# Performance work log

Hardware: AMD Instinct MI355X
Metric: run time of the kernel (lower is better)

The kernel has to match this reference:

```python
import jax, jax.numpy as jnp
import numpy as np


def setup_inputs() -> dict:
    key = jax.random.key(0)
    k1, k2 = jax.random.split(key)
    T, K, D = 100000, 512, 64
    flags_matrix = jax.random.uniform(k1, (T, K), dtype=jnp.float32)  # ~half > 0.5
    emb_weight = jax.random.normal(k2, (K, D), dtype=jnp.float32)
    return {"flags_matrix": flags_matrix, "emb_weight": emb_weight}


def reference(flags_matrix, emb_weight):
    # mask[t,k] = 1 if flag active; bag-of-embeddings mean over active items per row.
    mask = (flags_matrix > 0.5).astype(emb_weight.dtype)          # [T, K]
    counts = jnp.sum(mask, axis=1, keepdims=True)                  # [T, 1]
    sums = mask @ emb_weight                                       # [T, D] masked sum of embeddings
    # rows with no active flags -> zeros (matches the torch branch)
    return jnp.where(counts > 0, sums / jnp.maximum(counts, 1.0), 0.0)
```

## Files before the change

### kernel.cpp

```cpp
#include <hip/hip_runtime.h>
#include <stdint.h>


#define T_ROWS 100000
#define K_FLAGS 512
#define D_DIM 64
#define TILES (T_ROWS / 16)

typedef __attribute__((ext_vector_type(4))) float f32x4;
typedef __attribute__((ext_vector_type(8))) short bf16x8;

__device__ __forceinline__ uint32_t f32_to_bf16_rne(float f) {
  union { float f; uint32_t u; } v; v.f = f;
  uint32_t u = v.u;
  return (u + 0x7FFFu + ((u >> 16) & 1u)) >> 16;
}

__global__ __launch_bounds__(1024, 8) void flagbag_kernel(const float* __restrict__ flags,
                                                          const float* __restrict__ W,
                                                          float* __restrict__ out) {
  __shared__ uint4 sB[16 * 4 * 64];
  __shared__ uint32_t sM[16][256];

  const int tid  = threadIdx.x;
  const int lane = tid & 63;
  const int wave = tid >> 6;
  const int tile = wave * 512 + (int)blockIdx.x;
  const bool active = (tile < TILES);
  const int t0 = tile * 16;

  if (active) {
    const float* ft = flags + (size_t)t0 * K_FLAGS + lane * 8;

    uint32_t D0 = 0, D1 = 0, D2 = 0, D3 = 0;
    f32x4 ra[4], rb[4];
#pragma unroll
    for (int r = 0; r < 3; ++r) {
      ra[r] = *reinterpret_cast<const f32x4*>(ft + r * K_FLAGS);
      rb[r] = *reinterpret_cast<const f32x4*>(ft + r * K_FLAGS + 4);
    }
#pragma unroll
    for (int r = 0; r < 16; ++r) {
      if (r + 3 < 16) {
        ra[(r + 3) & 3] = *reinterpret_cast<const f32x4*>(ft + (r + 3) * K_FLAGS);
        rb[(r + 3) & 3] = *reinterpret_cast<const f32x4*>(ft + (r + 3) * K_FLAGS + 4);
      }
      const f32x4 a = ra[r & 3], b = rb[r & 3];
      uint32_t byte = 0;
#pragma unroll
      for (int j = 0; j < 4; ++j) {
        byte |= (a[j] > 0.5f) ? (1u << j)       : 0u;
        byte |= (b[j] > 0.5f) ? (1u << (j + 4)) : 0u;
      }
      const uint32_t sh = byte << ((r & 3) * 8);
      if ((r >> 2) == 0) D0 |= sh;
      else if ((r >> 2) == 1) D1 |= sh;
      else if ((r >> 2) == 2) D2 |= sh;
      else D3 |= sh;
    }

    uint32_t* sMw = sM[wave];
    sMw[0 * 64 + (lane ^ 0)]  = D0;
    sMw[1 * 64 + (lane ^ 4)]  = D1;
    sMw[2 * 64 + (lane ^ 8)]  = D2;
    sMw[3 * 64 + (lane ^ 12)] = D3;
  }

#pragma unroll
  for (int p = 0; p < 4; ++p) {
    const int E  = tid + p * 1024;
    const int s  = E >> 8;
    const int nt = (E >> 6) & 3;
    const int ln = E & 63;
    const int n  = (ln & 15) + 16 * nt;
    const int kq = ln >> 4;
    const int kb = 128 * kq + 8 * s;
    uint32_t r[4];
#pragma unroll
    for (int j = 0; j < 4; ++j) {
      uint32_t lo = f32_to_bf16_rne(W[(size_t)(kb + 2 * j    ) * D_DIM + n]);
      uint32_t hi = f32_to_bf16_rne(W[(size_t)(kb + 2 * j + 1) * D_DIM + n]);
      r[j] = lo | (hi << 16);
    }
    sB[E] = make_uint4(r[0], r[1], r[2], r[3]);
  }
  __syncthreads();

  if (!active) return;

  const int m  = lane & 15;
  const int kq = lane >> 4;
  const int mj = m >> 2, mb = m & 3;
  const uint8_t* sMb = reinterpret_cast<const uint8_t*>(sM[wave]);

  uint32_t mbytes[16];
#pragma unroll
  for (int s = 0; s < 16; ++s)
    mbytes[s] = sMb[(size_t)(mj * 64 + ((16 * kq + s) ^ (4 * mj))) * 4 + mb];

  int cnt = 0;
#pragma unroll
  for (int s = 0; s < 16; ++s) cnt += __popc(mbytes[s]);
  cnt += __shfl_xor(cnt, 16);
  cnt += __shfl_xor(cnt, 32);
  const float inv = (cnt > 0) ? (1.0f / (float)cnt) : 0.0f;

  const uint4* sbl = &sB[lane];
  f32x4 acc[4];
#pragma unroll
  for (int nt = 0; nt < 4; ++nt) acc[nt] = (f32x4){0.f, 0.f, 0.f, 0.f};

  uint4 bc[4], bn[4];
#pragma unroll
  for (int nt = 0; nt < 4; ++nt) bc[nt] = sbl[nt * 64];

#pragma unroll
  for (int s = 0; s < 16; ++s) {
    if (s + 1 < 16) {
#pragma unroll
      for (int nt = 0; nt < 4; ++nt) bn[nt] = sbl[((s + 1) * 4 + nt) * 64];
    }
    const uint32_t byte = mbytes[s];
    bf16x8 af;
#pragma unroll
    for (int e = 0; e < 8; ++e) af[e] = ((byte >> e) & 1u) ? (short)0x3F80 : (short)0;

#pragma unroll
    for (int nt = 0; nt < 4; ++nt)
      acc[nt] = __builtin_amdgcn_mfma_f32_16x16x32_bf16(
          af, *reinterpret_cast<const bf16x8*>(&bc[nt]), acc[nt], 0, 0, 0);

#pragma unroll
    for (int nt = 0; nt < 4; ++nt) bc[nt] = bn[nt];
  }

#pragma unroll
  for (int r = 0; r < 4; ++r) {
    const int row = kq * 4 + r;
    const float invr = __shfl(inv, row);
    float* orow = out + (size_t)(t0 + row) * D_DIM + m;
#pragma unroll
    for (int nt = 0; nt < 4; ++nt)
      orow[16 * nt] = acc[nt][r] * invr;
  }
}

extern "C" void kernel_launch(void* const* d_in, const int* in_sizes, int n_in,
                              void* d_out, int out_size, void* d_ws, size_t ws_size,
                              hipStream_t stream) {
  const float* flags = (const float*)d_in[0];
  const float* W     = (const float*)d_in[1];
  float* out         = (float*)d_out;

  hipLaunchKernelGGL(flagbag_kernel, dim3(512), dim3(1024), 0, stream, flags, W, out);
}
```

Before: 42.95 us.

## Switch to 32x32x16 MFMA with wave pairs sharing 32-row tiles

Replaces the per-wave 16-row tile computed with four 16x16x32 MFMAs per k-step with 32-row tiles split across wave pairs. Each wave builds masks for 16 rows, and each wave of the pair computes one 32-column half of the output using 32 steps of the 32x32x16 bf16 MFMA. This cuts per-wave accumulator registers and LDS B-fragment loads, and reorganises the swizzled shared mask and B layouts to match. Count reduction and output writes are remapped to the 32x32 accumulator layout. The trade-off is more serial MFMA steps per wave and shared dependence between waves of a pair through the mask buffer.

Measured after the change: 47.31 us. 1.1x slower.

```diff
diff --git a/kernel.cpp b/kernel.cpp
--- a/kernel.cpp
+++ b/kernel.cpp
@@ -5,10 +5,11 @@
 #define T_ROWS 100000
 #define K_FLAGS 512
 #define D_DIM 64
-#define TILES (T_ROWS / 16)
+#define TILES32 (T_ROWS / 32)
 
-typedef __attribute__((ext_vector_type(4))) float f32x4;
-typedef __attribute__((ext_vector_type(8))) short bf16x8;
+typedef __attribute__((ext_vector_type(4)))  float f32x4;
+typedef __attribute__((ext_vector_type(16))) float f32x16;
+typedef __attribute__((ext_vector_type(8)))  short bf16x8;
 
 __device__ __forceinline__ uint32_t f32_to_bf16_rne(float f) {
   union { float f; uint32_t u; } v; v.f = f;
@@ -19,18 +20,20 @@
 __global__ __launch_bounds__(1024, 8) void flagbag_kernel(const float* __restrict__ flags,
                                                           const float* __restrict__ W,
                                                           float* __restrict__ out) {
-  __shared__ uint4 sB[16 * 4 * 64];
-  __shared__ uint32_t sM[16][256];
+  __shared__ uint4 sB[32 * 2 * 64];
+  __shared__ uint32_t sM[8][512];
 
-  const int tid  = threadIdx.x;
-  const int lane = tid & 63;
-  const int wave = tid >> 6;
-  const int tile = wave * 512 + (int)blockIdx.x;
-  const bool active = (tile < TILES);
-  const int t0 = tile * 16;
+  const int tid   = threadIdx.x;
+  const int lane  = tid & 63;
+  const int wave  = tid >> 6;
+  const int pairv = wave >> 1;
+  const int mate  = wave & 1;
+  const int slot  = pairv * 512 + (int)blockIdx.x;
+  const bool active = (slot < TILES32);
+  const int t0 = (active ? slot : 0) * 32;
 
   if (active) {
-    const float* ft = flags + (size_t)t0 * K_FLAGS + lane * 8;
+    const float* ft = flags + (size_t)(t0 + 16 * mate) * K_FLAGS + lane * 8;
 
     uint32_t D0 = 0, D1 = 0, D2 = 0, D3 = 0;
     f32x4 ra[4], rb[4];
@@ -59,22 +62,22 @@
       else D3 |= sh;
     }
 
-    uint32_t* sMw = sM[wave];
-    sMw[0 * 64 + (lane ^ 0)]  = D0;
-    sMw[1 * 64 + (lane ^ 4)]  = D1;
-    sMw[2 * 64 + (lane ^ 8)]  = D2;
-    sMw[3 * 64 + (lane ^ 12)] = D3;
+    uint32_t* sMp = sM[pairv];
+    const int xr = 16 * mate;
+    sMp[mate * 256 + 0 * 64 + (lane ^ 0  ^ xr)] = D0;
+    sMp[mate * 256 + 1 * 64 + (lane ^ 4  ^ xr)] = D1;
+    sMp[mate * 256 + 2 * 64 + (lane ^ 8  ^ xr)] = D2;
+    sMp[mate * 256 + 3 * 64 + (lane ^ 12 ^ xr)] = D3;
   }
 
 #pragma unroll
   for (int p = 0; p < 4; ++p) {
-    const int E  = tid + p * 1024;
-    const int s  = E >> 8;
-    const int nt = (E >> 6) & 3;
-    const int ln = E & 63;
-    const int n  = (ln & 15) + 16 * nt;
-    const int kq = ln >> 4;
-    const int kb = 128 * kq + 8 * s;
+    const int E   = tid + p * 1024;
+    const int ln  = E & 63;
+    const int ntc = (E >> 6) & 1;
+    const int s   = E >> 7;
+    const int n   = (ln & 31) + 32 * ntc;
+    const int kb  = 16 * s + 8 * (ln >> 5);
     uint32_t r[4];
 #pragma unroll
     for (int j = 0; j < 4; ++j) {
@@ -85,63 +88,48 @@
     sB[E] = make_uint4(r[0], r[1], r[2], r[3]);
   }
   __syncthreads();
-
   if (!active) return;
 
-  const int m  = lane & 15;
-  const int kq = lane >> 4;
-  const int mj = m >> 2, mb = m & 3;
-  const uint8_t* sMb = reinterpret_cast<const uint8_t*>(sM[wave]);
+  const int lr     = lane & 31;
+  const int kg     = lane >> 5;
+  const int region = lr >> 4;
+  const int mj     = (lr & 15) >> 2;
+  const int mb     = lr & 3;
+  const int baseDw = region * 256 + mj * 64;
+  const int X      = (4 * mj) ^ (16 * region);
+  const uint8_t* sMb = reinterpret_cast<const uint8_t*>(sM[pairv]);
 
-  uint32_t mbytes[16];
+  f32x16 acc;
 #pragma unroll
-  for (int s = 0; s < 16; ++s)
-    mbytes[s] = sMb[(size_t)(mj * 64 + ((16 * kq + s) ^ (4 * mj))) * 4 + mb];
+  for (int i = 0; i < 16; ++i) acc[i] = 0.f;
+  int cnt = 0;
 
-  int cnt = 0;
+  uint4 bc = sB[mate * 64 + lane];
 #pragma unroll
-  for (int s = 0; s < 16; ++s) cnt += __popc(mbytes[s]);
-  cnt += __shfl_xor(cnt, 16);
-  cnt += __shfl_xor(cnt, 32);
-  const float inv = (cnt > 0) ? (1.0f / (float)cnt) : 0.0f;
+  for (int s = 0; s < 32; ++s) {
+    uint4 bn;
+    if (s + 1 < 32) bn = sB[(s + 1) * 128 + mate * 64 + lane];
 
-  const uint4* sbl = &sB[lane];
-  f32x4 acc[4];
-#pragma unroll
-  for (int nt = 0; nt < 4; ++nt) acc[nt] = (f32x4){0.f, 0.f, 0.f, 0.f};
+    const uint32_t byte = sMb[(size_t)(baseDw + ((2 * s + kg) ^ X)) * 4 + mb];
+    cnt += __popc(byte);
 
-  uint4 bc[4], bn[4];
-#pragma unroll
-  for (int nt = 0; nt < 4; ++nt) bc[nt] = sbl[nt * 64];
-
-#pragma unroll
-  for (int s = 0; s < 16; ++s) {
-    if (s + 1 < 16) {
-#pragma unroll
-      for (int nt = 0; nt < 4; ++nt) bn[nt] = sbl[((s + 1) * 4 + nt) * 64];
-    }
-    const uint32_t byte = mbytes[s];
     bf16x8 af;
 #pragma unroll
     for (int e = 0; e < 8; ++e) af[e] = ((byte >> e) & 1u) ? (short)0x3F80 : (short)0;
 
-#pragma unroll
-    for (int nt = 0; nt < 4; ++nt)
-      acc[nt] = __builtin_amdgcn_mfma_f32_16x16x32_bf16(
-          af, *reinterpret_cast<const bf16x8*>(&bc[nt]), acc[nt], 0, 0, 0);
+    acc = __builtin_amdgcn_mfma_f32_32x32x16_bf16(
+        af, *reinterpret_cast<const bf16x8*>(&bc), acc, 0, 0, 0);
+    bc = bn;
+  }
+
+  cnt += __shfl_xor(cnt, 32);
+  const float inv = (cnt > 0) ? (1.0f / (float)cnt) : 0.0f;
 
 #pragma unroll
-    for (int nt = 0; nt < 4; ++nt) bc[nt] = bn[nt];
-  }
-
-#pragma unroll
-  for (int r = 0; r < 4; ++r) {
-    const int row = kq * 4 + r;
+  for (int reg = 0; reg < 16; ++reg) {
+    const int row = (reg & 3) + 8 * (reg >> 2) + 4 * kg;
     const float invr = __shfl(inv, row);
-    float* orow = out + (size_t)(t0 + row) * D_DIM + m;
-#pragma unroll
-    for (int nt = 0; nt < 4; ++nt)
-      orow[16 * nt] = acc[nt][r] * invr;
+    out[(size_t)(t0 + row) * D_DIM + lr + 32 * mate] = acc[reg] * invr;
   }
 }
 
```

## Pair waves to share mask tiles and split output columns

Applied to the files above, without the earlier changes.

Waves are paired over a 32-row slot. Each wave still packs the flag bits for its own 16 rows. After the barrier, each wave computes both 16-row tiles but only half of the 64 output columns. This halves the per-wave LDS reads of the bf16 embedding fragments, at the cost of reading mask bytes from two LDS slabs and building two A fragments per step. Row counts are now accumulated inside the MFMA loop. The kernel reads about 200 MB of flags, so it is likely bound by HBM bandwidth, which caps any gain.

Result: slower. 47.85 us (+11.4%).

```diff
diff --git a/kernel.cpp b/kernel.cpp
--- a/kernel.cpp
+++ b/kernel.cpp
@@ -5,7 +5,7 @@
 #define T_ROWS 100000
 #define K_FLAGS 512
 #define D_DIM 64
-#define TILES (T_ROWS / 16)
+#define TILES32 (T_ROWS / 32)
 
 typedef __attribute__((ext_vector_type(4))) float f32x4;
 typedef __attribute__((ext_vector_type(8))) short bf16x8;
@@ -25,12 +25,14 @@
   const int tid  = threadIdx.x;
   const int lane = tid & 63;
   const int wave = tid >> 6;
-  const int tile = wave * 512 + (int)blockIdx.x;
-  const bool active = (tile < TILES);
-  const int t0 = tile * 16;
+  const int pair = wave >> 1;
+  const int mate = wave & 1;
+  const int slot = pair * 512 + (int)blockIdx.x;
+  const bool active = (slot < TILES32);
+  const int t0 = (active ? slot : 0) * 32;
 
   if (active) {
-    const float* ft = flags + (size_t)t0 * K_FLAGS + lane * 8;
+    const float* ft = flags + (size_t)(t0 + 16 * mate) * K_FLAGS + lane * 8;
 
     uint32_t D0 = 0, D1 = 0, D2 = 0, D3 = 0;
     f32x4 ra[4], rb[4];
@@ -73,8 +75,7 @@
     const int nt = (E >> 6) & 3;
     const int ln = E & 63;
     const int n  = (ln & 15) + 16 * nt;
-    const int kq = ln >> 4;
-    const int kb = 128 * kq + 8 * s;
+    const int kb = 128 * (ln >> 4) + 8 * s;
     uint32_t r[4];
 #pragma unroll
     for (int j = 0; j < 4; ++j) {
@@ -85,63 +86,70 @@
     sB[E] = make_uint4(r[0], r[1], r[2], r[3]);
   }
   __syncthreads();
-
   if (!active) return;
 
   const int m  = lane & 15;
   const int kq = lane >> 4;
   const int mj = m >> 2, mb = m & 3;
-  const uint8_t* sMb = reinterpret_cast<const uint8_t*>(sM[wave]);
+  const int m4 = 4 * mj;
+  const int C  = 4 * (mj * 64 + 16 * kq) + mb;
+  const uint8_t* sA0 = reinterpret_cast<const uint8_t*>(sM[pair * 2    ]);
+  const uint8_t* sA1 = reinterpret_cast<const uint8_t*>(sM[pair * 2 + 1]);
+  const int ntb = 2 * mate;
 
-  uint32_t mbytes[16];
-#pragma unroll
-  for (int s = 0; s < 16; ++s)
-    mbytes[s] = sMb[(size_t)(mj * 64 + ((16 * kq + s) ^ (4 * mj))) * 4 + mb];
+  f32x4 a00 = {0.f,0.f,0.f,0.f}, a01 = {0.f,0.f,0.f,0.f};
+  f32x4 a10 = {0.f,0.f,0.f,0.f}, a11 = {0.f,0.f,0.f,0.f};
+  int cntA = 0, cntB = 0;
 
-  int cnt = 0;
-#pragma unroll
-  for (int s = 0; s < 16; ++s) cnt += __popc(mbytes[s]);
-  cnt += __shfl_xor(cnt, 16);
-  cnt += __shfl_xor(cnt, 32);
-  const float inv = (cnt > 0) ? (1.0f / (float)cnt) : 0.0f;
-
-  const uint4* sbl = &sB[lane];
-  f32x4 acc[4];
-#pragma unroll
-  for (int nt = 0; nt < 4; ++nt) acc[nt] = (f32x4){0.f, 0.f, 0.f, 0.f};
-
-  uint4 bc[4], bn[4];
-#pragma unroll
-  for (int nt = 0; nt < 4; ++nt) bc[nt] = sbl[nt * 64];
+  uint4 bc0 = sB[ntb * 64 + lane];
+  uint4 bc1 = sB[(ntb + 1) * 64 + lane];
 
 #pragma unroll
   for (int s = 0; s < 16; ++s) {
+    uint4 bn0, bn1;
     if (s + 1 < 16) {
+      bn0 = sB[(s + 1) * 256 + ntb * 64 + lane];
+      bn1 = sB[(s + 1) * 256 + (ntb + 1) * 64 + lane];
+    }
+
+    const uint32_t byteA = sA0[C + 4 * (s ^ m4)];
+    const uint32_t byteB = sA1[C + 4 * (s ^ m4)];
+    cntA += __popc(byteA);
+    cntB += __popc(byteB);
+
+    bf16x8 afA, afB;
 #pragma unroll
-      for (int nt = 0; nt < 4; ++nt) bn[nt] = sbl[((s + 1) * 4 + nt) * 64];
+    for (int e = 0; e < 8; ++e) {
+      afA[e] = ((byteA >> e) & 1u) ? (short)0x3F80 : (short)0;
+      afB[e] = ((byteB >> e) & 1u) ? (short)0x3F80 : (short)0;
     }
-    const uint32_t byte = mbytes[s];
-    bf16x8 af;
-#pragma unroll
-    for (int e = 0; e < 8; ++e) af[e] = ((byte >> e) & 1u) ? (short)0x3F80 : (short)0;
 
-#pragma unroll
-    for (int nt = 0; nt < 4; ++nt)
-      acc[nt] = __builtin_amdgcn_mfma_f32_16x16x32_bf16(
-          af, *reinterpret_cast<const bf16x8*>(&bc[nt]), acc[nt], 0, 0, 0);
+    a00 = __builtin_amdgcn_mfma_f32_16x16x32_bf16(afA, *reinterpret_cast<const bf16x8*>(&bc0), a00, 0, 0, 0);
+    a01 = __builtin_amdgcn_mfma_f32_16x16x32_bf16(afA, *reinterpret_cast<const bf16x8*>(&bc1), a01, 0, 0, 0);
+    a10 = __builtin_amdgcn_mfma_f32_16x16x32_bf16(afB, *reinterpret_cast<const bf16x8*>(&bc0), a10, 0, 0, 0);
+    a11 = __builtin_amdgcn_mfma_f32_16x16x32_bf16(afB, *reinterpret_cast<const bf16x8*>(&bc1), a11, 0, 0, 0);
 
-#pragma unroll
-    for (int nt = 0; nt < 4; ++nt) bc[nt] = bn[nt];
+    bc0 = bn0; bc1 = bn1;
   }
+
+  cntA += __shfl_xor(cntA, 16);
+  cntA += __shfl_xor(cntA, 32);
+  cntB += __shfl_xor(cntB, 16);
+  cntB += __shfl_xor(cntB, 32);
+  const float invA = (cntA > 0) ? (1.0f / (float)cntA) : 0.0f;
+  const float invB = (cntB > 0) ? (1.0f / (float)cntB) : 0.0f;
 
 #pragma unroll
   for (int r = 0; r < 4; ++r) {
     const int row = kq * 4 + r;
-    const float invr = __shfl(inv, row);
-    float* orow = out + (size_t)(t0 + row) * D_DIM + m;
-#pragma unroll
-    for (int nt = 0; nt < 4; ++nt)
-      orow[16 * nt] = acc[nt][r] * invr;
+    const float invAr = __shfl(invA, row);
+    const float invBr = __shfl(invB, row);
+    float* orowA = out + (size_t)(t0 + row) * D_DIM + ntb * 16 + m;
+    float* orowB = out + (size_t)(t0 + 16 + row) * D_DIM + ntb * 16 + m;
+    orowA[0]  = a00[r] * invAr;
+    orowA[16] = a01[r] * invAr;
+    orowB[0]  = a10[r] * invBr;
+    orowB[16] = a11[r] * invBr;
   }
 }
 
```
